# Performance work log

Measured on AMD Instinct MI355X. Metric: run time of the kernel, lower is better.

Reference implementation:

```python
import jax, jax.numpy as jnp
import numpy as np

AUX_LOSS_WEIGHT = 0.01
TOP_K = 2


def setup_inputs() -> dict:
    key = jax.random.key(0)
    k0, k1, k2, k3, k4 = jax.random.split(key, 5)
    B, S, H, I, E = 4, 2048, 1024, 2816, 8
    scale = 0.02
    x = jax.random.normal(k0, (B, S, H), dtype=jnp.float32)
    Wr = jax.random.normal(k1, (H, E), dtype=jnp.float32) * scale   # router
    Wg = jax.random.normal(k2, (E, H, I), dtype=jnp.float32) * scale  # gate proj per expert
    Wu = jax.random.normal(k3, (E, H, I), dtype=jnp.float32) * scale  # up proj per expert
    Wd = jax.random.normal(k4, (E, I, H), dtype=jnp.float32) * scale  # down proj per expert
    return {"x": x, "Wr": Wr, "Wg": Wg, "Wu": Wu, "Wd": Wd}


def reference(x, Wr, Wg, Wu, Wd):
    B, S, H = x.shape
    E = Wr.shape[1]
    xf = x.reshape(-1, H)                      # [T, H]

    # Router: softmax -> top-k -> renormalize top-k weights
    logits = xf @ Wr                           # [T, E]
    probs = jax.nn.softmax(logits, axis=-1)
    vals, idx = jax.lax.top_k(probs, TOP_K)    # [T, K]
    vals = vals / (vals.sum(axis=-1, keepdims=True) + 1e-9)

    # Aux load-balancing loss (matches torch: mean prob * mean one-hot load)
    oh = jax.nn.one_hot(idx, E, dtype=xf.dtype)        # [T, K, E]
    expert_load = oh.sum(axis=1).mean(axis=0)          # [E]
    expert_prob = probs.mean(axis=0)                   # [E]
    router_loss = E * jnp.sum(expert_prob * expert_load) * AUX_LOSS_WEIGHT

    # Per-token combine weight for each expert: c[t,e] = sum_k vals[t,k] * (idx[t,k]==e)
    comb = jnp.einsum('tk,tke->te', vals, oh)          # [T, E]

    # Loop over the small fixed set of experts (dense SwiGLU, masked-weighted combine;
    # identical math to gather -> expert -> weighted index_add scatter)
    def expert_step(acc, ew):
        wg, wu, wd, ce = ew                            # [H,I], [H,I], [I,H], [T]
        h = jax.nn.silu(xf @ wg) * (xf @ wu)           # [T, I]
        return acc + (h @ wd) * ce[:, None], None

    out, _ = jax.lax.scan(expert_step, jnp.zeros_like(xf), (Wg, Wu, Wd, comb.T))
    return out.reshape(B, S, H), router_loss
```

## Files before the change

### kernel.cpp

```cpp
#include <hip/hip_runtime.h>
#include <stdint.h>

#define T_TOK 8192
#define HD    1024
#define ID    2816
#define NE    8
#define RCAP  17408
#define NYT   (RCAP / 128)

typedef __bf16 bf16x8 __attribute__((ext_vector_type(8)));
typedef float  f32x4  __attribute__((ext_vector_type(4)));

__device__ __forceinline__ unsigned short f2bf(float f) {
  union { float f; unsigned u; } v; v.f = f;
  unsigned r = v.u + 0x7FFFu + ((v.u >> 16) & 1u);
  return (unsigned short)(r >> 16);
}

__device__ __forceinline__ void gl16(const void* g, void* l) {
  __builtin_amdgcn_global_load_lds((__attribute__((address_space(1))) void*)g,
                                   (__attribute__((address_space(3))) void*)l,
                                   16, 0, 0);
}

__device__ __forceinline__ bf16x8 dsr128(unsigned a) {
  bf16x8 r;
  asm volatile("ds_read_b128 %0, %1" : "=v"(r) : "v"(a));
  return r;
}

#define S2VM(n) asm volatile("s_waitcnt vmcnt(" #n ")")
#define S2LG0   asm volatile("s_waitcnt lgkmcnt(0)")
#define SBAR0   __builtin_amdgcn_sched_barrier(0)
#define HBAR    __builtin_amdgcn_s_barrier()

__global__ void k_prep(const float* __restrict__ x, const float* __restrict__ Wr,
                       const float* __restrict__ Wg, const float* __restrict__ Wu,
                       const float* __restrict__ Wd,
                       unsigned short* __restrict__ Wgt, unsigned short* __restrict__ Wut,
                       unsigned short* __restrict__ Wdt, unsigned short* __restrict__ xb,
                       int* __restrict__ cnt, float* __restrict__ psum,
                       int* __restrict__ tok_e, float* __restrict__ tok_w) {
  __shared__ __align__(16) unsigned short tl[64 * 64];
  __shared__ float bp[NE];
  __shared__ int bc[NE];
  const int bid = blockIdx.x;
  const int t = threadIdx.x;

  if (bid < 16896) {
    const int m = bid / 704, bx = bid - m * 704;
    const float* src; unsigned short* dst; int R, C;
    if (m < 8)       { src = Wg + (size_t)m * HD * ID;        dst = Wgt + (size_t)m * HD * ID;        R = HD; C = ID; }
    else if (m < 16) { src = Wu + (size_t)(m - 8) * HD * ID;  dst = Wut + (size_t)(m - 8) * HD * ID;  R = HD; C = ID; }
    else             { src = Wd + (size_t)(m - 16) * HD * ID; dst = Wdt + (size_t)(m - 16) * HD * ID; R = ID; C = HD; }
    const int tc = C / 64;
    const int tr = bx / tc, tcc = bx % tc;
    const int r0 = tr * 64, c0 = tcc * 64;
    const int rb = t >> 4;
    const int c4 = t & 15;
    const float* sp = src + (size_t)(r0 + rb * 4) * C + c0 + c4 * 4;
    float4 v[4];
#pragma unroll
    for (int i = 0; i < 4; ++i) v[i] = *(const float4*)(sp + (size_t)i * C);
    const float* vf = (const float*)v;
#pragma unroll
    for (int q = 0; q < 4; ++q) {
      const int c = c4 * 4 + q;
      ushort4 o;
      o.x = f2bf(vf[0 * 4 + q]); o.y = f2bf(vf[1 * 4 + q]);
      o.z = f2bf(vf[2 * 4 + q]); o.w = f2bf(vf[3 * 4 + q]);
      *(ushort4*)&tl[c * 64 + ((rb ^ (c & 15)) * 4)] = o;
    }
    __syncthreads();
    const int orow = t >> 2, seg = t & 3;
    __align__(16) unsigned short tmp[16];
#pragma unroll
    for (int mI = 0; mI < 4; ++mI) {
      const int s = seg * 4 + mI;
      *(ushort4*)&tmp[mI * 4] = *(const ushort4*)&tl[orow * 64 + ((s ^ (orow & 15)) * 4)];
    }
    unsigned short* dp = dst + (size_t)(c0 + orow) * R + r0 + seg * 16;
    ((uint4*)dp)[0] = ((const uint4*)tmp)[0];
    ((uint4*)dp)[1] = ((const uint4*)tmp)[1];
  } else {
    const int b = bid - 16896;
    if (t < NE) { bp[t] = 0.f; bc[t] = 0; }
    __syncthreads();
    const int lane = t & 63, w = t >> 6;
    const int tok = b * 4 + w;
    float acc[NE] = {0.f, 0.f, 0.f, 0.f, 0.f, 0.f, 0.f, 0.f};
    for (int h = lane; h < HD; h += 64) {
      const float xv = x[(size_t)tok * HD + h];
      xb[(size_t)tok * HD + h] = f2bf(xv);
      const float4 w0 = *(const float4*)(Wr + h * 8);
      const float4 w1 = *(const float4*)(Wr + h * 8 + 4);
      acc[0] += xv * w0.x; acc[1] += xv * w0.y; acc[2] += xv * w0.z; acc[3] += xv * w0.w;
      acc[4] += xv * w1.x; acc[5] += xv * w1.y; acc[6] += xv * w1.z; acc[7] += xv * w1.w;
    }
#pragma unroll
    for (int e = 0; e < NE; ++e)
      for (int off = 32; off > 0; off >>= 1)
        acc[e] += __shfl_xor(acc[e], off, 64);
    if (lane == 0) {
      float mx = acc[0];
      for (int e = 1; e < NE; ++e) mx = fmaxf(mx, acc[e]);
      float p[NE], s = 0.f;
      for (int e = 0; e < NE; ++e) { p[e] = __expf(acc[e] - mx); s += p[e]; }
      const float inv = 1.f / s;
      for (int e = 0; e < NE; ++e) p[e] *= inv;
      int e0 = 0;
      for (int e = 1; e < NE; ++e) if (p[e] > p[e0]) e0 = e;
      int e1 = (e0 == 0) ? 1 : 0;
      for (int e = 0; e < NE; ++e) if (e != e0 && p[e] > p[e1]) e1 = e;
      const float v0 = p[e0], v1 = p[e1];
      const float invs = 1.f / (v0 + v1 + 1e-9f);
      tok_e[2 * tok] = e0;          tok_e[2 * tok + 1] = e1;
      tok_w[2 * tok] = v0 * invs;   tok_w[2 * tok + 1] = v1 * invs;
      atomicAdd(&bc[e0], 1); atomicAdd(&bc[e1], 1);
      for (int e = 0; e < NE; ++e) atomicAdd(&bp[e], p[e]);
    }
    __syncthreads();
    if (t < NE) { atomicAdd(&cnt[t], bc[t]); atomicAdd(&psum[t], bp[t]); }
  }
}

__global__ void k_offsets(const int* __restrict__ cnt, const float* __restrict__ psum,
                          int* __restrict__ offp, int* __restrict__ pair_tok,
                          float* __restrict__ pair_w, float* __restrict__ loss_out) {
  __shared__ int soff[NE + 1], scnt[NE];
  if (threadIdx.x == 0) {
    int o = 0;
    for (int e = 0; e < NE; ++e) {
      soff[e] = o; scnt[e] = cnt[e];
      o += (scnt[e] + 127) & ~127;
    }
    soff[NE] = o;
    for (int e = 0; e <= NE; ++e) offp[e] = soff[e];
    float loss = 0.f;
    for (int e = 0; e < NE; ++e) loss += psum[e] * (float)scnt[e];
    loss *= (float)NE * 0.01f / ((float)T_TOK * (float)T_TOK);
    *loss_out = loss;
  }
  __syncthreads();
  for (int e = 0; e < NE; ++e) {
    const int base = soff[e] + scnt[e];
    const int n = soff[e + 1] - base;
    for (int j = threadIdx.x; j < n; j += blockDim.x) {
      pair_tok[base + j] = -1;
      pair_w[base + j] = 0.f;
    }
  }
}

__global__ void k_scatter(const int* __restrict__ tok_e, const float* __restrict__ tok_w,
                          const int* __restrict__ offp, int* __restrict__ cursor,
                          int* __restrict__ pair_tok, float* __restrict__ pair_w,
                          int* __restrict__ inv_p) {
  const int t = blockIdx.x * 256 + threadIdx.x;
#pragma unroll
  for (int k = 0; k < 2; ++k) {
    const int e = tok_e[2 * t + k];
    const int pos = atomicAdd(&cursor[e], 1);
    const int idx = offp[e] + pos;
    pair_tok[idx] = t;
    pair_w[idx] = tok_w[2 * t + k];
    inv_p[2 * t + k] = idx;
  }
}

__launch_bounds__(256, 2)
__global__ void k_stage1(const unsigned short* __restrict__ xb,
                         const unsigned short* __restrict__ Wgt,
                         const unsigned short* __restrict__ Wut,
                         const int* __restrict__ offp,
                         const int* __restrict__ pair_tok,
                         unsigned short* __restrict__ act) {
  __shared__ __align__(16) unsigned short lA[8192];
  __shared__ __align__(16) unsigned short lBg[8192];
  __shared__ __align__(16) unsigned short lBu[8192];
  __shared__ int toks[128];

  const int row0 = blockIdx.y * 128;
  if (row0 >= offp[8]) return;
  int e = 0;
  while (offp[e + 1] <= row0) ++e;
  const int i0 = blockIdx.x * 128;
  const int tid = threadIdx.x;
  if (tid < 128) {
    const int tk = pair_tok[row0 + tid];
    toks[tid] = tk < 0 ? 0 : tk;
  }
  __syncthreads();

  const int lane = tid & 63, w = tid >> 6;
  const unsigned short* gA[4];
  const unsigned short* gBg[4];
  const unsigned short* gBu[4];
  unsigned ldso[4];
  const unsigned short* wgtE = Wgt + (size_t)e * ID * HD;
  const unsigned short* wutE = Wut + (size_t)e * ID * HD;
#pragma unroll
  for (int j = 0; j < 4; ++j) {
    const int row = (w * 4 + j) * 8 + (lane >> 3);
    const int kb = (lane & 7) ^ (row & 7);
    gA[j]  = xb + (size_t)toks[row] * HD + kb * 8;
    gBg[j] = wgtE + (size_t)(i0 + row) * HD + kb * 8;
    gBu[j] = wutE + (size_t)(i0 + row) * HD + kb * 8;
    ldso[j] = (unsigned)(w * 4 + j) * 512u;
  }

  const f32x4 zero = {0.f, 0.f, 0.f, 0.f};
  f32x4 accg[4][4], accu[4][4];
#pragma unroll
  for (int a = 0; a < 4; ++a)
#pragma unroll
    for (int b = 0; b < 4; ++b) { accg[a][b] = zero; accu[a][b] = zero; }

  const int wm = (w & 1) * 64, wn = (w >> 1) * 64;
  const int colm = lane & 15, quad = lane >> 4;

  for (int kt = 0; kt < HD / 64; ++kt) {
    __syncthreads();
    const int ko = kt * 64;
#pragma unroll
    for (int j = 0; j < 4; ++j) {
      gl16(gA[j] + ko,  &lA[ldso[j]]);
      gl16(gBg[j] + ko, &lBg[ldso[j]]);
      gl16(gBu[j] + ko, &lBu[ldso[j]]);
    }
    __syncthreads();
#pragma unroll
    for (int kk = 0; kk < 2; ++kk) {
      const int kbl = kk * 4 + quad;
      bf16x8 af[4], bg[4], bu[4];
#pragma unroll
      for (int mf = 0; mf < 4; ++mf) {
        const int r = wm + mf * 16 + colm;
        af[mf] = *(const bf16x8*)&lA[r * 64 + ((kbl ^ (r & 7)) * 8)];
      }
#pragma unroll
      for (int nf = 0; nf < 4; ++nf) {
        const int r = wn + nf * 16 + colm;
        const int o = r * 64 + ((kbl ^ (r & 7)) * 8);
        bg[nf] = *(const bf16x8*)&lBg[o];
        bu[nf] = *(const bf16x8*)&lBu[o];
      }
#pragma unroll
      for (int mf = 0; mf < 4; ++mf)
#pragma unroll
        for (int nf = 0; nf < 4; ++nf) {
          accg[mf][nf] = __builtin_amdgcn_mfma_f32_16x16x32_bf16(af[mf], bg[nf], accg[mf][nf], 0, 0, 0);
          accu[mf][nf] = __builtin_amdgcn_mfma_f32_16x16x32_bf16(af[mf], bu[nf], accu[mf][nf], 0, 0, 0);
        }
    }
  }

#pragma unroll
  for (int mf = 0; mf < 4; ++mf) {
#pragma unroll
    for (int r = 0; r < 4; ++r) {
      const int orow = row0 + wm + mf * 16 + quad * 4 + r;
      unsigned short* arow = act + (size_t)orow * ID + i0 + wn + colm;
#pragma unroll
      for (int nf = 0; nf < 4; ++nf) {
        const float g = accg[mf][nf][r];
        const float u = accu[mf][nf][r];
        const float h = (g / (1.f + __expf(-g))) * u;
        arow[nf * 16] = f2bf(h);
      }
    }
  }
}

#define STG2(b, h, t) do { \
  const int go_ = (t) * 64 + (h) * 32; \
  char* lb_ = (char*)smem + ((b) * 16384 + (h) * 8192) + wdst; \
  gl16(srcA0 + go_, lb_); \
  gl16(srcA1 + go_, lb_ + 4096); \
  gl16(srcB0 + go_, lb_ + 32768); \
  gl16(srcB1 + go_, lb_ + 32768 + 4096); \
} while (0)

#define S2_PHASE(b, h, STAGE, VMW) do { \
  bf16x8 af[4], bf_[4]; \
  _Pragma("unroll") for (int i_ = 0; i_ < 4; ++i_) \
    af[i_] = dsr128(aRd + (b) * 16384 + (h) * 8192 + i_ * 1024); \
  _Pragma("unroll") for (int i_ = 0; i_ < 4; ++i_) \
    bf_[i_] = dsr128(bRd + (b) * 16384 + (h) * 8192 + i_ * 1024); \
  STAGE; \
  SBAR0; HBAR; S2LG0; SBAR0; \
  __builtin_amdgcn_s_setprio(1); \
  _Pragma("unroll") for (int mf_ = 0; mf_ < 4; ++mf_) \
    _Pragma("unroll") for (int nf_ = 0; nf_ < 4; ++nf_) \
      acc[mf_][nf_] = __builtin_amdgcn_mfma_f32_16x16x32_bf16(af[mf_], bf_[nf_], acc[mf_][nf_], 0, 0, 0); \
  __builtin_amdgcn_s_setprio(0); \
  SBAR0; \
  VMW; \
  HBAR; \
} while (0)

__launch_bounds__(256, 2)
__global__ void k_stage2(const unsigned short* __restrict__ act,
                         const unsigned short* __restrict__ Wdt,
                         const int* __restrict__ offp,
                         float* __restrict__ contrib) {
  __shared__ __align__(16) unsigned short smem[32768];

  int wg = blockIdx.x;
  wg = (wg & 7) * 136 + (wg >> 3);
  const int htile = wg & 7, ytile = wg >> 3;
  const int row0 = ytile * 128;
  if (row0 >= offp[8]) return;
  int e = 0;
  while (offp[e + 1] <= row0) ++e;
  const int h0 = htile * 128;

  const int tid = threadIdx.x;
  const int l = tid & 63, w = tid >> 6;
  const int colm = l & 15, quad = l >> 4;
  const int wm = (w & 1) * 64, wn = (w >> 1) * 64;

  const int rr = w * 16 + (l >> 2);
  const int ks = (l & 3) ^ ((l >> 3) & 3);
  const unsigned short* wdE = Wdt + (size_t)e * HD * ID;
  const unsigned short* srcA0 = act + (size_t)(row0 + rr) * ID + ks * 8;
  const unsigned short* srcA1 = act + (size_t)(row0 + 64 + rr) * ID + ks * 8;
  const unsigned short* srcB0 = wdE + (size_t)(h0 + rr) * ID + ks * 8;
  const unsigned short* srcB1 = wdE + (size_t)(h0 + 64 + rr) * ID + ks * 8;
  const int wdst = w * 1024;

  const unsigned ldsBase =
      (unsigned)(uintptr_t)(__attribute__((address_space(3))) unsigned short*)smem;
  const int slotB = (quad ^ ((colm >> 1) & 3)) * 16;
  const unsigned aRd = ldsBase + (unsigned)((wm + colm) * 64 + slotB);
  const unsigned bRd = ldsBase + 32768u + (unsigned)((wn + colm) * 64 + slotB);

  const f32x4 zero = {0.f, 0.f, 0.f, 0.f};
  f32x4 acc[4][4];
#pragma unroll
  for (int a = 0; a < 4; ++a)
#pragma unroll
    for (int b = 0; b < 4; ++b) acc[a][b] = zero;

  STG2(0, 0, 0);
  STG2(0, 1, 0);
  STG2(1, 0, 1);
  S2VM(4); HBAR;

  for (int T = 0; T < 44; T += 2) {
    S2_PHASE(0, 0,
      { if (T + 1 < 44) STG2(1, 1, T + 1); },
      { if (T + 1 < 44) { S2VM(8); } else { S2VM(0); } });
    S2_PHASE(0, 1,
      { if (T + 2 < 44) STG2(0, 0, T + 2); },
      { if (T + 2 < 44) { S2VM(8); } else if (T + 1 < 44) { S2VM(4); } else { S2VM(0); } });
    S2_PHASE(1, 0,
      { if (T + 2 < 44) STG2(0, 1, T + 2); },
      { if (T + 2 < 44) { S2VM(8); } else { S2VM(0); } });
    S2_PHASE(1, 1,
      { if (T + 3 < 44) STG2(1, 0, T + 3); },
      { if (T + 3 < 44) { S2VM(8); } else if (T + 2 < 44) { S2VM(4); } else { S2VM(0); } });
  }

#pragma unroll
  for (int mf = 0; mf < 4; ++mf) {
#pragma unroll
    for (int r = 0; r < 4; ++r) {
      const int lrow = wm + mf * 16 + quad * 4 + r;
      float* crow = contrib + (size_t)(row0 + lrow) * HD + h0 + wn + colm;
#pragma unroll
      for (int nf = 0; nf < 4; ++nf)
        crow[nf * 16] = acc[mf][nf][r];
    }
  }
}

__global__ void k_combine(const float* __restrict__ contrib, const int* __restrict__ inv_p,
                          const float* __restrict__ tok_w, float* __restrict__ out) {
  const int t = blockIdx.x;
  const int h4 = threadIdx.x;
  const int p0 = inv_p[2 * t], p1 = inv_p[2 * t + 1];
  const float w0 = tok_w[2 * t], w1 = tok_w[2 * t + 1];
  const float4 a = ((const float4*)(contrib + (size_t)p0 * HD))[h4];
  const float4 b = ((const float4*)(contrib + (size_t)p1 * HD))[h4];
  float4 o;
  o.x = w0 * a.x + w1 * b.x;
  o.y = w0 * a.y + w1 * b.y;
  o.z = w0 * a.z + w1 * b.z;
  o.w = w0 * a.w + w1 * b.w;
  ((float4*)(out + (size_t)t * HD))[h4] = o;
}

extern "C" void kernel_launch(void* const* d_in, const int* in_sizes, int n_in,
                              void* d_out, int out_size, void* d_ws, size_t ws_size,
                              hipStream_t stream) {
  const float* x  = (const float*)d_in[0];
  const float* Wr = (const float*)d_in[1];
  const float* Wg = (const float*)d_in[2];
  const float* Wu = (const float*)d_in[3];
  const float* Wd = (const float*)d_in[4];
  float* out = (float*)d_out;

  char* ws = (char*)d_ws;
  const size_t off_xb  = 256;
  const size_t sz_xb   = (size_t)T_TOK * HD * 2;
  const size_t sz_w    = (size_t)NE * HD * ID * 2;
  const size_t off_wgt = off_xb + sz_xb;
  const size_t off_wut = off_wgt + sz_w;
  const size_t off_wdt = off_wut + sz_w;
  const size_t off_act = off_wdt + sz_w;
  const size_t sz_act  = (size_t)RCAP * ID * 2;
  const size_t off_ptk = off_act + sz_act;
  const size_t off_pw  = off_ptk + (size_t)RCAP * 4;
  const size_t off_te  = off_pw + (size_t)RCAP * 4;
  const size_t off_tw  = off_te + (size_t)T_TOK * 2 * 4;
  const size_t off_ip  = off_tw + (size_t)T_TOK * 2 * 4;
  const size_t need    = off_ip + (size_t)T_TOK * 2 * 4;
  if (ws_size < need) return;

  int*   cnt    = (int*)(ws + 0);
  float* psum   = (float*)(ws + 32);
  int*   cursor = (int*)(ws + 64);
  int*   offp   = (int*)(ws + 96);
  unsigned short* xb  = (unsigned short*)(ws + off_xb);
  unsigned short* Wgt = (unsigned short*)(ws + off_wgt);
  unsigned short* Wut = (unsigned short*)(ws + off_wut);
  unsigned short* Wdt = (unsigned short*)(ws + off_wdt);
  unsigned short* act = (unsigned short*)(ws + off_act);
  int*   pair_tok = (int*)(ws + off_ptk);
  float* pair_w   = (float*)(ws + off_pw);
  int*   tok_e    = (int*)(ws + off_te);
  float* tok_w    = (float*)(ws + off_tw);
  int*   inv_p    = (int*)(ws + off_ip);
  float* contrib  = (float*)(ws + off_wgt);

  hipMemsetAsync(ws, 0, 256, stream);

  k_prep<<<16896 + T_TOK / 4, 256, 0, stream>>>(x, Wr, Wg, Wu, Wd, Wgt, Wut, Wdt, xb,
                                                cnt, psum, tok_e, tok_w);
  k_offsets<<<1, 256, 0, stream>>>(cnt, psum, offp, pair_tok, pair_w, out + (size_t)T_TOK * HD);
  k_scatter<<<T_TOK / 256, 256, 0, stream>>>(tok_e, tok_w, offp, cursor, pair_tok, pair_w, inv_p);
  k_stage1<<<dim3(ID / 128, NYT), 256, 0, stream>>>(xb, Wgt, Wut, offp, pair_tok, act);
  k_stage2<<<NYT * (HD / 128), 256, 0, stream>>>(act, Wdt, offp, contrib);
  k_combine<<<T_TOK, 256, 0, stream>>>(contrib, inv_p, tok_w, out);
}
```

Before: 791.1 us.

## Pipeline stage1 gate/up GEMM with 512-thread blocks and double-buffered LDS

Rewrites the stage1 gate/up GEMM to use 512 threads, with 8 waves split so half compute the gate product and half compute the up product, halving accumulator registers per wave. Global-to-LDS loads are double-buffered in half-K phases with fine-grained vmcnt waits and priority hints, so loads overlap MFMA work. Gate results are exchanged through LDS for the SwiGLU epilogue. This reduces stalls from synchronous load/barrier patterns at the cost of one resident block per CU and an extra LDS round trip in the epilogue.

```diff
diff --git a/kernel.cpp b/kernel.cpp
--- a/kernel.cpp
+++ b/kernel.cpp
@@ -168,105 +168,132 @@
   }
 }
 
-__launch_bounds__(256, 2)
+#define A1_OFF(b,h)  ((b) * 16384 + (h) * 8192)
+#define B1G_OFF(b,h) (32768 + (b) * 16384 + (h) * 8192)
+#define B1U_OFF(b,h) (65536 + (b) * 16384 + (h) * 8192)
+
+#define STG1(b, h, t) do { \
+  const int go_ = (t) * 64 + (h) * 32; \
+  gl16(srcA + go_,  (char*)smem1 + A1_OFF(b,h)  + wdst); \
+  gl16(srcBg + go_, (char*)smem1 + B1G_OFF(b,h) + wdst); \
+  gl16(srcBu + go_, (char*)smem1 + B1U_OFF(b,h) + wdst); \
+} while (0)
+
+#define S1_PHASE(b, h, STAGE, VMW) do { \
+  bf16x8 af[4], bfr[4]; \
+  _Pragma("unroll") for (int i_ = 0; i_ < 4; ++i_) \
+    af[i_] = dsr128(aRd + A1_OFF(b,h) + i_ * 1024); \
+  _Pragma("unroll") for (int i_ = 0; i_ < 4; ++i_) \
+    bfr[i_] = dsr128(bRd + (b) * 16384 + (h) * 8192 + i_ * 1024); \
+  STAGE; \
+  SBAR0; HBAR; S2LG0; SBAR0; \
+  __builtin_amdgcn_s_setprio(1); \
+  _Pragma("unroll") for (int mf_ = 0; mf_ < 4; ++mf_) \
+    _Pragma("unroll") for (int nf_ = 0; nf_ < 4; ++nf_) \
+      acc[mf_][nf_] = __builtin_amdgcn_mfma_f32_16x16x32_bf16(af[mf_], bfr[nf_], acc[mf_][nf_], 0, 0, 0); \
+  __builtin_amdgcn_s_setprio(0); \
+  SBAR0; \
+  VMW; \
+  HBAR; \
+} while (0)
+
+__launch_bounds__(512, 1)
 __global__ void k_stage1(const unsigned short* __restrict__ xb,
                          const unsigned short* __restrict__ Wgt,
                          const unsigned short* __restrict__ Wut,
                          const int* __restrict__ offp,
                          const int* __restrict__ pair_tok,
                          unsigned short* __restrict__ act) {
-  __shared__ __align__(16) unsigned short lA[8192];
-  __shared__ __align__(16) unsigned short lBg[8192];
-  __shared__ __align__(16) unsigned short lBu[8192];
-  __shared__ int toks[128];
+  __shared__ __align__(16) unsigned short smem1[49152];
 
   const int row0 = blockIdx.y * 128;
   if (row0 >= offp[8]) return;
   int e = 0;
   while (offp[e + 1] <= row0) ++e;
   const int i0 = blockIdx.x * 128;
+
   const int tid = threadIdx.x;
-  if (tid < 128) {
-    const int tk = pair_tok[row0 + tid];
-    toks[tid] = tk < 0 ? 0 : tk;
-  }
-  __syncthreads();
-
-  const int lane = tid & 63, w = tid >> 6;
-  const unsigned short* gA[4];
-  const unsigned short* gBg[4];
-  const unsigned short* gBu[4];
-  unsigned ldso[4];
+  const int l = tid & 63, w = tid >> 6;
+  const int colm = l & 15, quad = l >> 4;
+  const int wm = (w & 1) * 64, wn = ((w >> 1) & 1) * 64;
+  const int mat = w >> 2;
+
+  const int rr = w * 16 + (l >> 2);
+  const int ks = (l & 3) ^ ((l >> 3) & 3);
+  int tk = pair_tok[row0 + rr];
+  if (tk < 0) tk = 0;
+  const unsigned short* srcA = xb + (size_t)tk * HD + ks * 8;
   const unsigned short* wgtE = Wgt + (size_t)e * ID * HD;
   const unsigned short* wutE = Wut + (size_t)e * ID * HD;
-#pragma unroll
-  for (int j = 0; j < 4; ++j) {
-    const int row = (w * 4 + j) * 8 + (lane >> 3);
-    const int kb = (lane & 7) ^ (row & 7);
-    gA[j]  = xb + (size_t)toks[row] * HD + kb * 8;
-    gBg[j] = wgtE + (size_t)(i0 + row) * HD + kb * 8;
-    gBu[j] = wutE + (size_t)(i0 + row) * HD + kb * 8;
-    ldso[j] = (unsigned)(w * 4 + j) * 512u;
-  }
+  const unsigned short* srcBg = wgtE + (size_t)(i0 + rr) * HD + ks * 8;
+  const unsigned short* srcBu = wutE + (size_t)(i0 + rr) * HD + ks * 8;
+  const int wdst = w * 1024;
+
+  const unsigned ldsBase =
+      (unsigned)(uintptr_t)(__attribute__((address_space(3))) unsigned short*)smem1;
+  const int slotB = (quad ^ ((colm >> 1) & 3)) * 16;
+  const unsigned aRd = ldsBase + (unsigned)((wm + colm) * 64 + slotB);
+  const unsigned bRd = ldsBase + 32768u + (unsigned)mat * 32768u
+                       + (unsigned)((wn + colm) * 64 + slotB);
 
   const f32x4 zero = {0.f, 0.f, 0.f, 0.f};
-  f32x4 accg[4][4], accu[4][4];
+  f32x4 acc[4][4];
 #pragma unroll
   for (int a = 0; a < 4; ++a)
 #pragma unroll
-    for (int b = 0; b < 4; ++b) { accg[a][b] = zero; accu[a][b] = zero; }
-
-  const int wm = (w & 1) * 64, wn = (w >> 1) * 64;
-  const int colm = lane & 15, quad = lane >> 4;
-
-  for (int kt = 0; kt < HD / 64; ++kt) {
-    __syncthreads();
-    const int ko = kt * 64;
-#pragma unroll
-    for (int j = 0; j < 4; ++j) {
-      gl16(gA[j] + ko,  &lA[ldso[j]]);
-      gl16(gBg[j] + ko, &lBg[ldso[j]]);
-      gl16(gBu[j] + ko, &lBu[ldso[j]]);
-    }
-    __syncthreads();
-#pragma unroll
-    for (int kk = 0; kk < 2; ++kk) {
-      const int kbl = kk * 4 + quad;
-      bf16x8 af[4], bg[4], bu[4];
-#pragma unroll
-      for (int mf = 0; mf < 4; ++mf) {
-        const int r = wm + mf * 16 + colm;
-        af[mf] = *(const bf16x8*)&lA[r * 64 + ((kbl ^ (r & 7)) * 8)];
+    for (int b = 0; b < 4; ++b) acc[a][b] = zero;
+
+  STG1(0, 0, 0);
+  STG1(0, 1, 0);
+  STG1(1, 0, 1);
+  S2VM(3); HBAR;
+
+  for (int T = 0; T < 16; T += 2) {
+    S1_PHASE(0, 0,
+      { if (T + 1 < 16) STG1(1, 1, T + 1); },
+      { if (T + 1 < 16) { S2VM(6); } else { S2VM(0); } });
+    S1_PHASE(0, 1,
+      { if (T + 2 < 16) STG1(0, 0, T + 2); },
+      { if (T + 2 < 16) { S2VM(6); } else if (T + 1 < 16) { S2VM(3); } else { S2VM(0); } });
+    S1_PHASE(1, 0,
+      { if (T + 2 < 16) STG1(0, 1, T + 2); },
+      { if (T + 2 < 16) { S2VM(6); } else { S2VM(0); } });
+    S1_PHASE(1, 1,
+      { if (T + 3 < 16) STG1(1, 0, T + 3); },
+      { if (T + 3 < 16) { S2VM(6); } else if (T + 2 < 16) { S2VM(3); } else { S2VM(0); } });
+  }
+
+  asm volatile("" ::: "memory");
+  __syncthreads();
+  float* sf = (float*)smem1;
+  const int qw = w & 3;
+  if (w < 4) {
+#pragma unroll
+    for (int mf = 0; mf < 4; ++mf)
+#pragma unroll
+      for (int r = 0; r < 4; ++r) {
+        const int rl = mf * 16 + quad * 4 + r;
+#pragma unroll
+        for (int nf = 0; nf < 4; ++nf)
+          sf[qw * 4352 + rl * 68 + nf * 16 + colm] = acc[mf][nf][r];
       }
-#pragma unroll
-      for (int nf = 0; nf < 4; ++nf) {
-        const int r = wn + nf * 16 + colm;
-        const int o = r * 64 + ((kbl ^ (r & 7)) * 8);
-        bg[nf] = *(const bf16x8*)&lBg[o];
-        bu[nf] = *(const bf16x8*)&lBu[o];
-      }
-#pragma unroll
-      for (int mf = 0; mf < 4; ++mf)
+  }
+  __syncthreads();
+  if (w >= 4) {
+#pragma unroll
+    for (int mf = 0; mf < 4; ++mf) {
+#pragma unroll
+      for (int r = 0; r < 4; ++r) {
+        const int rl = mf * 16 + quad * 4 + r;
+        const int orow = row0 + wm + rl;
+        unsigned short* arow = act + (size_t)orow * ID + i0 + wn + colm;
 #pragma unroll
         for (int nf = 0; nf < 4; ++nf) {
-          accg[mf][nf] = __builtin_amdgcn_mfma_f32_16x16x32_bf16(af[mf], bg[nf], accg[mf][nf], 0, 0, 0);
-          accu[mf][nf] = __builtin_amdgcn_mfma_f32_16x16x32_bf16(af[mf], bu[nf], accu[mf][nf], 0, 0, 0);
+          const float g = sf[qw * 4352 + rl * 68 + nf * 16 + colm];
+          const float u = acc[mf][nf][r];
+          const float h = (g / (1.f + __expf(-g))) * u;
+          arow[nf * 16] = f2bf(h);
         }
-    }
-  }
-
-#pragma unroll
-  for (int mf = 0; mf < 4; ++mf) {
-#pragma unroll
-    for (int r = 0; r < 4; ++r) {
-      const int orow = row0 + wm + mf * 16 + quad * 4 + r;
-      unsigned short* arow = act + (size_t)orow * ID + i0 + wn + colm;
-#pragma unroll
-      for (int nf = 0; nf < 4; ++nf) {
-        const float g = accg[mf][nf][r];
-        const float u = accu[mf][nf][r];
-        const float h = (g / (1.f + __expf(-g))) * u;
-        arow[nf * 16] = f2bf(h);
       }
     }
   }
@@ -440,7 +467,7 @@
                                                 cnt, psum, tok_e, tok_w);
   k_offsets<<<1, 256, 0, stream>>>(cnt, psum, offp, pair_tok, pair_w, out + (size_t)T_TOK * HD);
   k_scatter<<<T_TOK / 256, 256, 0, stream>>>(tok_e, tok_w, offp, cursor, pair_tok, pair_w, inv_p);
-  k_stage1<<<dim3(ID / 128, NYT), 256, 0, stream>>>(xb, Wgt, Wut, offp, pair_tok, act);
+  k_stage1<<<dim3(ID / 128, NYT), 512, 0, stream>>>(xb, Wgt, Wut, offp, pair_tok, act);
   k_stage2<<<NYT * (HD / 128), 256, 0, stream>>>(act, Wdt, offp, contrib);
   k_combine<<<T_TOK, 256, 0, stream>>>(contrib, inv_p, tok_w, out);
 }
```

New measurement: 843.0 us. 1.07x slower.
